# Optimization experiments

Measured on AMD Instinct MI355X. Metric: run time of the kernel, lower is better.

## Reference

```python
import jax, jax.numpy as jnp
import numpy as np

N = 50000      # nodes
E = 800000     # edges (before self loops)
D_IN = 128
HID = 64
HEADS = 8
D_OUT = 10


def setup_inputs() -> dict:
    key = jax.random.key(0)
    ks = jax.random.split(key, 16)
    sc = 0.05
    x = jax.random.normal(ks[0], (N, D_IN), dtype=jnp.float32)
    edge_index = jax.random.randint(ks[1], (2, E), 0, N, dtype=jnp.int64)
    return {
        "x": x,
        "edge_index": edge_index,
        "W1": jax.random.normal(ks[2], (HEADS * HID, D_IN), dtype=jnp.float32) * sc,
        "a1_src": jax.random.normal(ks[3], (HEADS, HID), dtype=jnp.float32) * sc,
        "a1_dst": jax.random.normal(ks[4], (HEADS, HID), dtype=jnp.float32) * sc,
        "b1": jnp.zeros((HEADS * HID,), jnp.float32),
        "W2": jax.random.normal(ks[5], (HID, HEADS * HID), dtype=jnp.float32) * sc,
        "a2_src": jax.random.normal(ks[6], (1, HID), dtype=jnp.float32) * sc,
        "a2_dst": jax.random.normal(ks[7], (1, HID), dtype=jnp.float32) * sc,
        "b2": jnp.zeros((HID,), jnp.float32),
        "W3": jax.random.normal(ks[8], (HID, HID), dtype=jnp.float32) * sc,
        "a3_src": jax.random.normal(ks[9], (1, HID), dtype=jnp.float32) * sc,
        "a3_dst": jax.random.normal(ks[10], (1, HID), dtype=jnp.float32) * sc,
        "b3": jnp.zeros((HID,), jnp.float32),
        "Wc": jax.random.normal(ks[11], (D_OUT, HID), dtype=jnp.float32) * sc,
        "bc": jnp.zeros((D_OUT,), jnp.float32),
    }


def gat_conv(x, src, dst, W, a_src, a_dst, b, concat):
    """PyG GATConv (eval mode, add_self_loops already applied to src/dst)."""
    heads, out_ch = a_src.shape
    n = x.shape[0]
    h = (x @ W.T).reshape(n, heads, out_ch)          # [N, H, C]
    a_s = jnp.einsum('nhc,hc->nh', h, a_src)          # [N, H]
    a_d = jnp.einsum('nhc,hc->nh', h, a_dst)          # [N, H]
    e = jax.nn.leaky_relu(a_s[src] + a_d[dst], 0.2)   # [Etot, H]
    # segment softmax over incoming edges of each destination node
    m = jax.ops.segment_max(e, dst, num_segments=n)
    ex = jnp.exp(e - m[dst])
    s = jax.ops.segment_sum(ex, dst, num_segments=n)
    alpha = ex / (s[dst] + 1e-16)                     # [Etot, H]
    out = jax.ops.segment_sum(h[src] * alpha[:, :, None], dst, num_segments=n)
    if concat:
        out = out.reshape(n, heads * out_ch)
    else:
        out = out.mean(axis=1)
    return out + b


def reference(x, edge_index, W1, a1_src, a1_dst, b1, W2, a2_src, a2_dst, b2,
              W3, a3_src, a3_dst, b3, Wc, bc):
    loops = jnp.arange(N, dtype=edge_index.dtype)
    src = jnp.concatenate([edge_index[0], loops])
    dst = jnp.concatenate([edge_index[1], loops])
    h = jax.nn.elu(gat_conv(x, src, dst, W1, a1_src, a1_dst, b1, True))
    h = jax.nn.elu(gat_conv(h, src, dst, W2, a2_src, a2_dst, b2, False))
    h = jax.nn.elu(gat_conv(h, src, dst, W3, a3_src, a3_dst, b3, False))
    return h @ Wc.T + bc
```

## Files before the change

### kernel.cpp

```cpp
#include <hip/hip_runtime.h>
#include <math.h>

#define N_NODES 50000
#define N_EDGES 800000
#define ETOT    (N_EDGES + N_NODES)

typedef short bf16x8 __attribute__((ext_vector_type(8)));
typedef float f32x4  __attribute__((ext_vector_type(4)));

__device__ __forceinline__ float b2f(unsigned int u16) {
    return __uint_as_float(u16 << 16);
}
__device__ __forceinline__ unsigned short f2b(float f) {
    unsigned int u = __float_as_uint(f);
    u += 0x7fffu + ((u >> 16) & 1u);
    return (unsigned short)(u >> 16);
}
__device__ __forceinline__ void unpack8(uint4 v, float* f) {
    f[0] = __uint_as_float(v.x << 16); f[1] = __uint_as_float(v.x & 0xffff0000u);
    f[2] = __uint_as_float(v.y << 16); f[3] = __uint_as_float(v.y & 0xffff0000u);
    f[4] = __uint_as_float(v.z << 16); f[5] = __uint_as_float(v.z & 0xffff0000u);
    f[6] = __uint_as_float(v.w << 16); f[7] = __uint_as_float(v.w & 0xffff0000u);
}

__global__ __launch_bounds__(256) void k_prep(const float* __restrict__ w1,
                                              const float* __restrict__ w2,
                                              const float* __restrict__ w3,
                                              unsigned short* __restrict__ o1,
                                              unsigned short* __restrict__ o2,
                                              unsigned short* __restrict__ o3,
                                              int* __restrict__ deg,
                                              int* __restrict__ flag) {
    int i = blockIdx.x * 256 + threadIdx.x;
    if (i < N_NODES) deg[i] = 0;
    if (i == 0) *flag = 0;
    if (i < 512 * 128 / 4) {
        float4 v = ((const float4*)w1)[i];
        ushort2* o = (ushort2*)(o1 + i * 4);
        o[0] = make_ushort2(f2b(v.x), f2b(v.y));
        o[1] = make_ushort2(f2b(v.z), f2b(v.w));
    }
    if (i < 64 * 512 / 4) {
        float4 v = ((const float4*)w2)[i];
        ushort2* o = (ushort2*)(o2 + i * 4);
        o[0] = make_ushort2(f2b(v.x), f2b(v.y));
        o[1] = make_ushort2(f2b(v.z), f2b(v.w));
    }
    if (i < 64 * 64 / 4) {
        float4 v = ((const float4*)w3)[i];
        ushort2* o = (ushort2*)(o3 + i * 4);
        o[0] = make_ushort2(f2b(v.x), f2b(v.y));
        o[1] = make_ushort2(f2b(v.z), f2b(v.w));
    }
}

__global__ void k_detect(const int* __restrict__ idx, int* __restrict__ flag) {
    int i = blockIdx.x * blockDim.x + threadIdx.x;
    int v = idx[2 * i + 1];
    unsigned long long any = __ballot(v != 0);
    if ((threadIdx.x & 63) == 0 && any) atomicOr(flag, 1);
}

__device__ __forceinline__ int edge_src(const int* idx, int e, int is32) {
    return is32 ? idx[e] : idx[2 * e];
}
__device__ __forceinline__ int edge_dst(const int* idx, int e, int is32) {
    return is32 ? idx[N_EDGES + e] : idx[2 * (N_EDGES + e)];
}

__global__ void k_degree(const int* __restrict__ idx, const int* __restrict__ flag,
                         int* __restrict__ deg) {
    int e = blockIdx.x * blockDim.x + threadIdx.x;
    if (e >= ETOT) return;
    int is32 = *flag;
    int d = (e < N_EDGES) ? edge_dst(idx, e, is32) : (e - N_EDGES);
    atomicAdd(&deg[d], 1);
}

__global__ __launch_bounds__(256) void k_scan1(const int* __restrict__ deg,
                                               int* __restrict__ rowptr,
                                               int* __restrict__ bsum) {
    __shared__ int sd[256];
    int t = threadIdx.x;
    int i = blockIdx.x * 256 + t;
    int v = (i < N_NODES) ? deg[i] : 0;
    sd[t] = v;
    __syncthreads();
#pragma unroll
    for (int off = 1; off < 256; off <<= 1) {
        int a = (t >= off) ? sd[t - off] : 0;
        __syncthreads();
        sd[t] += a;
        __syncthreads();
    }
    if (i < N_NODES) rowptr[i] = sd[t] - v;
    if (t == 255) bsum[blockIdx.x] = sd[255];
}

__global__ __launch_bounds__(256) void k_scan2(int* __restrict__ bsum,
                                               int* __restrict__ boff,
                                               int* __restrict__ rowptr,
                                               int nb) {
    __shared__ int sd[256];
    int t = threadIdx.x;
    int v = (t < nb) ? bsum[t] : 0;
    sd[t] = v;
    __syncthreads();
#pragma unroll
    for (int off = 1; off < 256; off <<= 1) {
        int a = (t >= off) ? sd[t - off] : 0;
        __syncthreads();
        sd[t] += a;
        __syncthreads();
    }
    boff[t] = sd[t] - v;
    if (t == 255) rowptr[N_NODES] = sd[255];
}

__global__ __launch_bounds__(256) void k_scan3(int* __restrict__ rowptr,
                                               const int* __restrict__ boff,
                                               int* __restrict__ cursor) {
    int i = blockIdx.x * 256 + threadIdx.x;
    if (i >= N_NODES) return;
    int r = rowptr[i] + boff[blockIdx.x];
    rowptr[i] = r;
    cursor[i] = r;
}

__global__ void k_scatter(const int* __restrict__ idx, const int* __restrict__ flag,
                          int* __restrict__ cursor, int* __restrict__ col) {
    int e = blockIdx.x * blockDim.x + threadIdx.x;
    if (e >= ETOT) return;
    int is32 = *flag;
    int s, d;
    if (e < N_EDGES) { s = edge_src(idx, e, is32); d = edge_dst(idx, e, is32); }
    else             { s = d = e - N_EDGES; }
    int pos = atomicAdd(&cursor[d], 1);
    col[pos] = s;
}

template<int AFP32>
__global__ __launch_bounds__(256) void k_gemm(const float* __restrict__ Af,
                                              const unsigned short* __restrict__ Ab,
                                              const unsigned short* __restrict__ W,
                                              unsigned short* __restrict__ C,
                                              const float* __restrict__ a_src,
                                              const float* __restrict__ a_dst,
                                              float* __restrict__ asb,
                                              float* __restrict__ adb,
                                              int M, int K, int Nout, int Hstr) {
    __shared__ unsigned short As[64 * 40];
    __shared__ unsigned short Bs[64 * 40];
    __shared__ float red_s[4][64];
    __shared__ float red_d[4][64];
    int t = threadIdx.x;
    int w = t >> 6, l = t & 63;
    int quad = l >> 4, lm = l & 15;
    int m0 = blockIdx.y * 64, n0 = blockIdx.x * 64;
    int hd = blockIdx.x;
    int lr = t >> 2;
    int lc = (t & 3) * 8;

    f32x4 acc[4];
#pragma unroll
    for (int r = 0; r < 4; ++r) acc[r] = (f32x4){0.f, 0.f, 0.f, 0.f};

    for (int k0 = 0; k0 < K; k0 += 32) {
        int m = m0 + lr;
        if (AFP32) {
            float4 a0 = {0.f,0.f,0.f,0.f}, a1 = {0.f,0.f,0.f,0.f};
            if (m < M) {
                const float4* ap = (const float4*)(Af + (size_t)m * K + k0 + lc);
                a0 = ap[0]; a1 = ap[1];
            }
            unsigned int u0 = (unsigned int)f2b(a0.x) | ((unsigned int)f2b(a0.y) << 16);
            unsigned int u1 = (unsigned int)f2b(a0.z) | ((unsigned int)f2b(a0.w) << 16);
            unsigned int u2 = (unsigned int)f2b(a1.x) | ((unsigned int)f2b(a1.y) << 16);
            unsigned int u3 = (unsigned int)f2b(a1.z) | ((unsigned int)f2b(a1.w) << 16);
            *(uint4*)&As[lr * 40 + lc] = make_uint4(u0, u1, u2, u3);
        } else {
            uint4 av = make_uint4(0, 0, 0, 0);
            if (m < M) av = *(const uint4*)(Ab + (size_t)m * K + k0 + lc);
            *(uint4*)&As[lr * 40 + lc] = av;
        }
        uint4 bv = *(const uint4*)(W + (size_t)(n0 + lr) * K + k0 + lc);
        *(uint4*)&Bs[lr * 40 + lc] = bv;
        __syncthreads();

        bf16x8 bfrag = *(const bf16x8*)&Bs[(w * 16 + lm) * 40 + quad * 8];
#pragma unroll
        for (int r = 0; r < 4; ++r) {
            bf16x8 afrag = *(const bf16x8*)&As[(r * 16 + lm) * 40 + quad * 8];
            acc[r] = __builtin_amdgcn_mfma_f32_16x16x32_bf16(afrag, bfrag, acc[r], 0, 0, 0);
        }
        __syncthreads();
    }

#pragma unroll
    for (int r = 0; r < 4; ++r)
#pragma unroll
        for (int g = 0; g < 4; ++g) {
            int m = m0 + r * 16 + quad * 4 + g;
            if (m < M) C[(size_t)m * Nout + n0 + w * 16 + lm] = f2b(acc[r][g]);
        }

    float as = a_src[hd * 64 + w * 16 + lm];
    float ad = a_dst[hd * 64 + w * 16 + lm];
#pragma unroll
    for (int r = 0; r < 4; ++r) {
#pragma unroll
        for (int g = 0; g < 4; ++g) {
            float vs = acc[r][g] * as;
            float vd = acc[r][g] * ad;
#pragma unroll
            for (int off = 1; off < 16; off <<= 1) {
                vs += __shfl_xor(vs, off);
                vd += __shfl_xor(vd, off);
            }
            if (lm == 0) {
                red_s[w][r * 16 + quad * 4 + g] = vs;
                red_d[w][r * 16 + quad * 4 + g] = vd;
            }
        }
    }
    __syncthreads();
    if (t < 64) {
        float vs = red_s[0][t] + red_s[1][t] + red_s[2][t] + red_s[3][t];
        float vd = red_d[0][t] + red_d[1][t] + red_d[2][t] + red_d[3][t];
        int m = m0 + t;
        if (m < M) {
            asb[(size_t)m * Hstr + hd] = vs;
            adb[(size_t)m * Hstr + hd] = vd;
        }
    }
}

__global__ __launch_bounds__(256) void k_agg8(const unsigned short* __restrict__ h,
                                              const float* __restrict__ asrc,
                                              const float* __restrict__ adst,
                                              const int* __restrict__ rowptr,
                                              const int* __restrict__ col,
                                              const float* __restrict__ bias,
                                              unsigned short* __restrict__ out) {
    int n = blockIdx.x * 4 + (threadIdx.x >> 6);
    if (n >= N_NODES) return;
    int l = threadIdx.x & 63;
    int j = l >> 3;
    int start = rowptr[n], end = rowptr[n + 1];
    float adn = adst[n * 8 + j];

    float ssum = 0.f;
    float o[8] = {0.f, 0.f, 0.f, 0.f, 0.f, 0.f, 0.f, 0.f};
    int k = start;
    for (; k + 4 <= end; k += 4) {
        int s0 = col[k], s1 = col[k + 1], s2 = col[k + 2], s3 = col[k + 3];
        float t0 = asrc[s0 * 8 + j], t1 = asrc[s1 * 8 + j];
        float t2 = asrc[s2 * 8 + j], t3 = asrc[s3 * 8 + j];
        uint4 hv0 = *(const uint4*)(h + (size_t)s0 * 512 + l * 8);
        uint4 hv1 = *(const uint4*)(h + (size_t)s1 * 512 + l * 8);
        uint4 hv2 = *(const uint4*)(h + (size_t)s2 * 512 + l * 8);
        uint4 hv3 = *(const uint4*)(h + (size_t)s3 * 512 + l * 8);
        float f[8];
        float e0 = t0 + adn; e0 = (e0 > 0.f) ? e0 : 0.2f * e0;
        float ex0 = __expf(e0); ssum += ex0;
        unpack8(hv0, f);
#pragma unroll
        for (int i = 0; i < 8; ++i) o[i] += ex0 * f[i];
        float e1 = t1 + adn; e1 = (e1 > 0.f) ? e1 : 0.2f * e1;
        float ex1 = __expf(e1); ssum += ex1;
        unpack8(hv1, f);
#pragma unroll
        for (int i = 0; i < 8; ++i) o[i] += ex1 * f[i];
        float e2 = t2 + adn; e2 = (e2 > 0.f) ? e2 : 0.2f * e2;
        float ex2 = __expf(e2); ssum += ex2;
        unpack8(hv2, f);
#pragma unroll
        for (int i = 0; i < 8; ++i) o[i] += ex2 * f[i];
        float e3 = t3 + adn; e3 = (e3 > 0.f) ? e3 : 0.2f * e3;
        float ex3 = __expf(e3); ssum += ex3;
        unpack8(hv3, f);
#pragma unroll
        for (int i = 0; i < 8; ++i) o[i] += ex3 * f[i];
    }
    for (; k < end; ++k) {
        int s = col[k];
        float e = asrc[s * 8 + j] + adn;
        e = (e > 0.f) ? e : 0.2f * e;
        float ex = __expf(e);
        ssum += ex;
        uint4 hv = *(const uint4*)(h + (size_t)s * 512 + l * 8);
        float f[8];
        unpack8(hv, f);
#pragma unroll
        for (int i = 0; i < 8; ++i) o[i] += ex * f[i];
    }
    float inv = 1.f / (ssum + 1e-16f);
    unsigned int p[4];
#pragma unroll
    for (int i = 0; i < 4; ++i) {
        float v0 = o[2 * i] * inv + bias[l * 8 + 2 * i];
        float v1 = o[2 * i + 1] * inv + bias[l * 8 + 2 * i + 1];
        v0 = (v0 > 0.f) ? v0 : expm1f(v0);
        v1 = (v1 > 0.f) ? v1 : expm1f(v1);
        p[i] = (unsigned int)f2b(v0) | ((unsigned int)f2b(v1) << 16);
    }
    *(uint4*)(out + (size_t)n * 512 + l * 8) = make_uint4(p[0], p[1], p[2], p[3]);
}

__global__ __launch_bounds__(256) void k_agg1(const unsigned short* __restrict__ h,
                                              const float* __restrict__ asrc,
                                              const float* __restrict__ adst,
                                              const int* __restrict__ rowptr,
                                              const int* __restrict__ col,
                                              const float* __restrict__ bias,
                                              unsigned short* __restrict__ out) {
    int n = blockIdx.x * 4 + (threadIdx.x >> 6);
    if (n >= N_NODES) return;
    int l = threadIdx.x & 63;
    int start = rowptr[n], end = rowptr[n + 1];
    float adn = adst[n];

    float ssum = 0.f, o = 0.f;
    int k = start;
    for (; k + 4 <= end; k += 4) {
        int s0 = col[k], s1 = col[k + 1], s2 = col[k + 2], s3 = col[k + 3];
        float t0 = asrc[s0], t1 = asrc[s1], t2 = asrc[s2], t3 = asrc[s3];
        unsigned short q0 = h[(size_t)s0 * 64 + l];
        unsigned short q1 = h[(size_t)s1 * 64 + l];
        unsigned short q2 = h[(size_t)s2 * 64 + l];
        unsigned short q3 = h[(size_t)s3 * 64 + l];
        float e0 = t0 + adn; e0 = (e0 > 0.f) ? e0 : 0.2f * e0;
        float ex0 = __expf(e0); ssum += ex0; o += ex0 * b2f(q0);
        float e1 = t1 + adn; e1 = (e1 > 0.f) ? e1 : 0.2f * e1;
        float ex1 = __expf(e1); ssum += ex1; o += ex1 * b2f(q1);
        float e2 = t2 + adn; e2 = (e2 > 0.f) ? e2 : 0.2f * e2;
        float ex2 = __expf(e2); ssum += ex2; o += ex2 * b2f(q2);
        float e3 = t3 + adn; e3 = (e3 > 0.f) ? e3 : 0.2f * e3;
        float ex3 = __expf(e3); ssum += ex3; o += ex3 * b2f(q3);
    }
    for (; k < end; ++k) {
        int s = col[k];
        float e = asrc[s] + adn;
        e = (e > 0.f) ? e : 0.2f * e;
        float ex = __expf(e);
        ssum += ex;
        o += ex * b2f(h[(size_t)s * 64 + l]);
    }
    float v = o / (ssum + 1e-16f) + bias[l];
    v = (v > 0.f) ? v : expm1f(v);
    out[(size_t)n * 64 + l] = f2b(v);
}

__global__ __launch_bounds__(256) void k_classifier(const unsigned short* __restrict__ h,
                                                    const float* __restrict__ Wc,
                                                    const float* __restrict__ bc,
                                                    float* __restrict__ out) {
    __shared__ float sW[640];
    for (int i = threadIdx.x; i < 640; i += blockDim.x) sW[i] = Wc[i];
    __syncthreads();
    int idx = blockIdx.x * blockDim.x + threadIdx.x;
    if (idx >= N_NODES * 10) return;
    int n = idx / 10, d = idx - n * 10;
    const unsigned short* hr = h + (size_t)n * 64;
    const float* wr = sW + d * 64;
    float acc = 0.f;
#pragma unroll
    for (int c = 0; c < 64; ++c) acc += b2f(hr[c]) * wr[c];
    out[idx] = acc + bc[d];
}

extern "C" void kernel_launch(void* const* d_in, const int* in_sizes, int n_in,
                              void* d_out, int out_size, void* d_ws, size_t ws_size,
                              hipStream_t stream) {
    const float* x    = (const float*)d_in[0];
    const int*   eidx = (const int*)  d_in[1];
    const float* W1   = (const float*)d_in[2];
    const float* a1s  = (const float*)d_in[3];
    const float* a1d  = (const float*)d_in[4];
    const float* b1   = (const float*)d_in[5];
    const float* W2   = (const float*)d_in[6];
    const float* a2s  = (const float*)d_in[7];
    const float* a2d  = (const float*)d_in[8];
    const float* b2   = (const float*)d_in[9];
    const float* W3   = (const float*)d_in[10];
    const float* a3s  = (const float*)d_in[11];
    const float* a3d  = (const float*)d_in[12];
    const float* b3   = (const float*)d_in[13];
    const float* Wc   = (const float*)d_in[14];
    const float* bc   = (const float*)d_in[15];
    float* out = (float*)d_out;

    float* asbuf = (float*)d_ws;
    float* adbuf = asbuf + (size_t)N_NODES * 8;
    unsigned short* h1  = (unsigned short*)(adbuf + (size_t)N_NODES * 8);
    unsigned short* x2  = h1  + (size_t)N_NODES * 512;
    unsigned short* h2  = x2  + (size_t)N_NODES * 512;
    unsigned short* x3  = h2  + (size_t)N_NODES * 64;
    unsigned short* h3  = x3  + (size_t)N_NODES * 64;
    unsigned short* x4  = h3  + (size_t)N_NODES * 64;
    unsigned short* W1b = x4  + (size_t)N_NODES * 64;
    unsigned short* W2b = W1b + 512 * 128;
    unsigned short* W3b = W2b + 64 * 512;
    int* ibase  = (int*)(W3b + 64 * 64);
    int* deg    = ibase;
    int* flag   = deg + N_NODES;
    int* rowptr = flag + 1;
    int* cursor = rowptr + N_NODES + 1;
    int* bsum   = cursor + N_NODES;
    int* boff   = bsum + 256;
    int* col    = boff + 256;

    dim3 blk(256);
    const int SCAN_BLOCKS = (N_NODES + 255) / 256;

    k_prep<<<SCAN_BLOCKS, blk, 0, stream>>>(W1, W2, W3, W1b, W2b, W3b, deg, flag);
    k_detect<<<32, blk, 0, stream>>>(eidx, flag);
    k_degree<<<(ETOT + 255) / 256, blk, 0, stream>>>(eidx, flag, deg);
    k_scan1<<<SCAN_BLOCKS, blk, 0, stream>>>(deg, rowptr, bsum);
    k_scan2<<<1, blk, 0, stream>>>(bsum, boff, rowptr, SCAN_BLOCKS);
    k_scan3<<<SCAN_BLOCKS, blk, 0, stream>>>(rowptr, boff, cursor);
    k_scatter<<<(ETOT + 255) / 256, blk, 0, stream>>>(eidx, flag, cursor, col);

    int mblocks = (N_NODES + 63) / 64;
    int nblocks = N_NODES / 4;

    k_gemm<1><<<dim3(8, mblocks), blk, 0, stream>>>(x, (const unsigned short*)0, W1b, h1,
                                                    a1s, a1d, asbuf, adbuf,
                                                    N_NODES, 128, 512, 8);
    k_agg8<<<nblocks, blk, 0, stream>>>(h1, asbuf, adbuf, rowptr, col, b1, x2);

    k_gemm<0><<<dim3(1, mblocks), blk, 0, stream>>>((const float*)0, x2, W2b, h2,
                                                    a2s, a2d, asbuf, adbuf,
                                                    N_NODES, 512, 64, 1);
    k_agg1<<<nblocks, blk, 0, stream>>>(h2, asbuf, adbuf, rowptr, col, b2, x3);

    k_gemm<0><<<dim3(1, mblocks), blk, 0, stream>>>((const float*)0, x3, W3b, h3,
                                                    a3s, a3d, asbuf, adbuf,
                                                    N_NODES, 64, 64, 1);
    k_agg1<<<nblocks, blk, 0, stream>>>(h3, asbuf, adbuf, rowptr, col, b3, x4);

    k_classifier<<<(N_NODES * 10 + 255) / 256, blk, 0, stream>>>(x4, Wc, bc, out);
}
```

Before: 507.5 us.

## Pre-convert x to bf16, vectorize col loads, use packed FMA in aggregation

The input features are converted to bf16 once in the prep kernel, so the first GEMM reads bf16 instead of converting fp32 on the fly across 8 column blocks. The aggregation kernels now align the edge loop and load column indices as int4 with a one-step prefetch, use 32-bit unsigned index arithmetic, and use fmaxf for leaky-relu. The 8-head aggregation accumulates with v_pk_fma_f32 inline asm. These target gather latency and ALU work in the memory-bound aggregation, at the cost of an extra bf16 copy of x in the workspace and a larger prep launch.

Result: no change. 512.7 us (+1.0%).

```diff
diff --git a/kernel.cpp b/kernel.cpp
--- a/kernel.cpp
+++ b/kernel.cpp
@@ -7,6 +7,7 @@
 
 typedef short bf16x8 __attribute__((ext_vector_type(8)));
 typedef float f32x4  __attribute__((ext_vector_type(4)));
+typedef float f32x2  __attribute__((ext_vector_type(2)));
 
 __device__ __forceinline__ float b2f(unsigned int u16) {
     return __uint_as_float(u16 << 16);
@@ -16,16 +17,12 @@
     u += 0x7fffu + ((u >> 16) & 1u);
     return (unsigned short)(u >> 16);
 }
-__device__ __forceinline__ void unpack8(uint4 v, float* f) {
-    f[0] = __uint_as_float(v.x << 16); f[1] = __uint_as_float(v.x & 0xffff0000u);
-    f[2] = __uint_as_float(v.y << 16); f[3] = __uint_as_float(v.y & 0xffff0000u);
-    f[4] = __uint_as_float(v.z << 16); f[5] = __uint_as_float(v.z & 0xffff0000u);
-    f[6] = __uint_as_float(v.w << 16); f[7] = __uint_as_float(v.w & 0xffff0000u);
-}
-
-__global__ __launch_bounds__(256) void k_prep(const float* __restrict__ w1,
+
+__global__ __launch_bounds__(256) void k_prep(const float* __restrict__ x,
+                                              const float* __restrict__ w1,
                                               const float* __restrict__ w2,
                                               const float* __restrict__ w3,
+                                              unsigned short* __restrict__ xb,
                                               unsigned short* __restrict__ o1,
                                               unsigned short* __restrict__ o2,
                                               unsigned short* __restrict__ o3,
@@ -51,6 +48,15 @@
         ushort2* o = (ushort2*)(o3 + i * 4);
         o[0] = make_ushort2(f2b(v.x), f2b(v.y));
         o[1] = make_ushort2(f2b(v.z), f2b(v.w));
+    }
+    if (i < N_NODES * 128 / 8) {
+        const float4* xp = (const float4*)x + (size_t)i * 2;
+        float4 v0 = xp[0], v1 = xp[1];
+        unsigned int u0 = (unsigned int)f2b(v0.x) | ((unsigned int)f2b(v0.y) << 16);
+        unsigned int u1 = (unsigned int)f2b(v0.z) | ((unsigned int)f2b(v0.w) << 16);
+        unsigned int u2 = (unsigned int)f2b(v1.x) | ((unsigned int)f2b(v1.y) << 16);
+        unsigned int u3 = (unsigned int)f2b(v1.z) | ((unsigned int)f2b(v1.w) << 16);
+        *(uint4*)(xb + (size_t)i * 8) = make_uint4(u0, u1, u2, u3);
     }
 }
 
@@ -235,6 +241,24 @@
     }
 }
 
+__device__ __forceinline__ void agg8_acc(float t, float adn, uint4 hv,
+                                         float& ssum, f32x2* o2) {
+    float e = t + adn;
+    e = fmaxf(e, 0.2f * e);
+    float ex = __expf(e);
+    ssum += ex;
+    f32x2 ex2 = {ex, ex};
+    f32x2 f;
+    f.x = __uint_as_float(hv.x << 16); f.y = __uint_as_float(hv.x & 0xffff0000u);
+    asm("v_pk_fma_f32 %0, %1, %2, %0" : "+v"(o2[0]) : "v"(f), "v"(ex2));
+    f.x = __uint_as_float(hv.y << 16); f.y = __uint_as_float(hv.y & 0xffff0000u);
+    asm("v_pk_fma_f32 %0, %1, %2, %0" : "+v"(o2[1]) : "v"(f), "v"(ex2));
+    f.x = __uint_as_float(hv.z << 16); f.y = __uint_as_float(hv.z & 0xffff0000u);
+    asm("v_pk_fma_f32 %0, %1, %2, %0" : "+v"(o2[2]) : "v"(f), "v"(ex2));
+    f.x = __uint_as_float(hv.w << 16); f.y = __uint_as_float(hv.w & 0xffff0000u);
+    asm("v_pk_fma_f32 %0, %1, %2, %0" : "+v"(o2[3]) : "v"(f), "v"(ex2));
+}
+
 __global__ __launch_bounds__(256) void k_agg8(const unsigned short* __restrict__ h,
                                               const float* __restrict__ asrc,
                                               const float* __restrict__ adst,
@@ -246,65 +270,62 @@
     if (n >= N_NODES) return;
     int l = threadIdx.x & 63;
     int j = l >> 3;
+    int lbase = l << 3;
     int start = rowptr[n], end = rowptr[n + 1];
-    float adn = adst[n * 8 + j];
+    float adn = adst[(n << 3) + j];
 
     float ssum = 0.f;
-    float o[8] = {0.f, 0.f, 0.f, 0.f, 0.f, 0.f, 0.f, 0.f};
+    f32x2 o2[4];
+#pragma unroll
+    for (int i = 0; i < 4; ++i) o2[i] = (f32x2){0.f, 0.f};
+
     int k = start;
-    for (; k + 4 <= end; k += 4) {
-        int s0 = col[k], s1 = col[k + 1], s2 = col[k + 2], s3 = col[k + 3];
-        float t0 = asrc[s0 * 8 + j], t1 = asrc[s1 * 8 + j];
-        float t2 = asrc[s2 * 8 + j], t3 = asrc[s3 * 8 + j];
-        uint4 hv0 = *(const uint4*)(h + (size_t)s0 * 512 + l * 8);
-        uint4 hv1 = *(const uint4*)(h + (size_t)s1 * 512 + l * 8);
-        uint4 hv2 = *(const uint4*)(h + (size_t)s2 * 512 + l * 8);
-        uint4 hv3 = *(const uint4*)(h + (size_t)s3 * 512 + l * 8);
-        float f[8];
-        float e0 = t0 + adn; e0 = (e0 > 0.f) ? e0 : 0.2f * e0;
-        float ex0 = __expf(e0); ssum += ex0;
-        unpack8(hv0, f);
-#pragma unroll
-        for (int i = 0; i < 8; ++i) o[i] += ex0 * f[i];
-        float e1 = t1 + adn; e1 = (e1 > 0.f) ? e1 : 0.2f * e1;
-        float ex1 = __expf(e1); ssum += ex1;
-        unpack8(hv1, f);
-#pragma unroll
-        for (int i = 0; i < 8; ++i) o[i] += ex1 * f[i];
-        float e2 = t2 + adn; e2 = (e2 > 0.f) ? e2 : 0.2f * e2;
-        float ex2 = __expf(e2); ssum += ex2;
-        unpack8(hv2, f);
-#pragma unroll
-        for (int i = 0; i < 8; ++i) o[i] += ex2 * f[i];
-        float e3 = t3 + adn; e3 = (e3 > 0.f) ? e3 : 0.2f * e3;
-        float ex3 = __expf(e3); ssum += ex3;
-        unpack8(hv3, f);
-#pragma unroll
-        for (int i = 0; i < 8; ++i) o[i] += ex3 * f[i];
+    int kA = (start + 3) & ~3;
+    if (kA > end) kA = end;
+    for (; k < kA; ++k) {
+        int s = col[k];
+        float t = asrc[((unsigned)s << 3) + (unsigned)j];
+        uint4 hv = *(const uint4*)(h + ((unsigned)s << 9) + (unsigned)lbase);
+        agg8_acc(t, adn, hv, ssum, o2);
+    }
+    int kEnd4 = kA + ((end - kA) & ~3);
+    if (k < kEnd4) {
+        int4 cN = *(const int4*)(col + k);
+        for (; k < kEnd4; k += 4) {
+            int4 c = cN;
+            if (k + 8 <= kEnd4) cN = *(const int4*)(col + k + 4);
+            float t0 = asrc[((unsigned)c.x << 3) + (unsigned)j];
+            float t1 = asrc[((unsigned)c.y << 3) + (unsigned)j];
+            float t2 = asrc[((unsigned)c.z << 3) + (unsigned)j];
+            float t3 = asrc[((unsigned)c.w << 3) + (unsigned)j];
+            uint4 hv0 = *(const uint4*)(h + ((unsigned)c.x << 9) + (unsigned)lbase);
+            uint4 hv1 = *(const uint4*)(h + ((unsigned)c.y << 9) + (unsigned)lbase);
+            uint4 hv2 = *(const uint4*)(h + ((unsigned)c.z << 9) + (unsigned)lbase);
+            uint4 hv3 = *(const uint4*)(h + ((unsigned)c.w << 9) + (unsigned)lbase);
+            agg8_acc(t0, adn, hv0, ssum, o2);
+            agg8_acc(t1, adn, hv1, ssum, o2);
+            agg8_acc(t2, adn, hv2, ssum, o2);
+            agg8_acc(t3, adn, hv3, ssum, o2);
+        }
     }
     for (; k < end; ++k) {
         int s = col[k];
-        float e = asrc[s * 8 + j] + adn;
-        e = (e > 0.f) ? e : 0.2f * e;
-        float ex = __expf(e);
-        ssum += ex;
-        uint4 hv = *(const uint4*)(h + (size_t)s * 512 + l * 8);
-        float f[8];
-        unpack8(hv, f);
-#pragma unroll
-        for (int i = 0; i < 8; ++i) o[i] += ex * f[i];
-    }
+        float t = asrc[((unsigned)s << 3) + (unsigned)j];
+        uint4 hv = *(const uint4*)(h + ((unsigned)s << 9) + (unsigned)lbase);
+        agg8_acc(t, adn, hv, ssum, o2);
+    }
+
     float inv = 1.f / (ssum + 1e-16f);
     unsigned int p[4];
 #pragma unroll
     for (int i = 0; i < 4; ++i) {
-        float v0 = o[2 * i] * inv + bias[l * 8 + 2 * i];
-        float v1 = o[2 * i + 1] * inv + bias[l * 8 + 2 * i + 1];
+        float v0 = o2[i].x * inv + bias[lbase + 2 * i];
+        float v1 = o2[i].y * inv + bias[lbase + 2 * i + 1];
         v0 = (v0 > 0.f) ? v0 : expm1f(v0);
         v1 = (v1 > 0.f) ? v1 : expm1f(v1);
         p[i] = (unsigned int)f2b(v0) | ((unsigned int)f2b(v1) << 16);
     }
-    *(uint4*)(out + (size_t)n * 512 + l * 8) = make_uint4(p[0], p[1], p[2], p[3]);
+    *(uint4*)(out + (size_t)n * 512 + lbase) = make_uint4(p[0], p[1], p[2], p[3]);
 }
 
 __global__ __launch_bounds__(256) void k_agg1(const unsigned short* __restrict__ h,
@@ -322,29 +343,44 @@
 
     float ssum = 0.f, o = 0.f;
     int k = start;
-    for (; k + 4 <= end; k += 4) {
-        int s0 = col[k], s1 = col[k + 1], s2 = col[k + 2], s3 = col[k + 3];
-        float t0 = asrc[s0], t1 = asrc[s1], t2 = asrc[s2], t3 = asrc[s3];
-        unsigned short q0 = h[(size_t)s0 * 64 + l];
-        unsigned short q1 = h[(size_t)s1 * 64 + l];
-        unsigned short q2 = h[(size_t)s2 * 64 + l];
-        unsigned short q3 = h[(size_t)s3 * 64 + l];
-        float e0 = t0 + adn; e0 = (e0 > 0.f) ? e0 : 0.2f * e0;
-        float ex0 = __expf(e0); ssum += ex0; o += ex0 * b2f(q0);
-        float e1 = t1 + adn; e1 = (e1 > 0.f) ? e1 : 0.2f * e1;
-        float ex1 = __expf(e1); ssum += ex1; o += ex1 * b2f(q1);
-        float e2 = t2 + adn; e2 = (e2 > 0.f) ? e2 : 0.2f * e2;
-        float ex2 = __expf(e2); ssum += ex2; o += ex2 * b2f(q2);
-        float e3 = t3 + adn; e3 = (e3 > 0.f) ? e3 : 0.2f * e3;
-        float ex3 = __expf(e3); ssum += ex3; o += ex3 * b2f(q3);
+    int kA = (start + 3) & ~3;
+    if (kA > end) kA = end;
+    for (; k < kA; ++k) {
+        int s = col[k];
+        float t = asrc[s];
+        float hf = b2f(h[((unsigned)s << 6) + (unsigned)l]);
+        float e = t + adn; e = fmaxf(e, 0.2f * e);
+        float ex = __expf(e);
+        ssum += ex; o += ex * hf;
+    }
+    int kEnd4 = kA + ((end - kA) & ~3);
+    if (k < kEnd4) {
+        int4 cN = *(const int4*)(col + k);
+        for (; k < kEnd4; k += 4) {
+            int4 c = cN;
+            if (k + 8 <= kEnd4) cN = *(const int4*)(col + k + 4);
+            float t0 = asrc[c.x], t1 = asrc[c.y], t2 = asrc[c.z], t3 = asrc[c.w];
+            unsigned short q0 = h[((unsigned)c.x << 6) + (unsigned)l];
+            unsigned short q1 = h[((unsigned)c.y << 6) + (unsigned)l];
+            unsigned short q2 = h[((unsigned)c.z << 6) + (unsigned)l];
+            unsigned short q3 = h[((unsigned)c.w << 6) + (unsigned)l];
+            float e0 = t0 + adn; e0 = fmaxf(e0, 0.2f * e0);
+            float ex0 = __expf(e0); ssum += ex0; o += ex0 * b2f(q0);
+            float e1 = t1 + adn; e1 = fmaxf(e1, 0.2f * e1);
+            float ex1 = __expf(e1); ssum += ex1; o += ex1 * b2f(q1);
+            float e2 = t2 + adn; e2 = fmaxf(e2, 0.2f * e2);
+            float ex2 = __expf(e2); ssum += ex2; o += ex2 * b2f(q2);
+            float e3 = t3 + adn; e3 = fmaxf(e3, 0.2f * e3);
+            float ex3 = __expf(e3); ssum += ex3; o += ex3 * b2f(q3);
+        }
     }
     for (; k < end; ++k) {
         int s = col[k];
-        float e = asrc[s] + adn;
-        e = (e > 0.f) ? e : 0.2f * e;
+        float t = asrc[s];
+        float hf = b2f(h[((unsigned)s << 6) + (unsigned)l]);
+        float e = t + adn; e = fmaxf(e, 0.2f * e);
         float ex = __expf(e);
-        ssum += ex;
-        o += ex * b2f(h[(size_t)s * 64 + l]);
+        ssum += ex; o += ex * hf;
     }
     float v = o / (ssum + 1e-16f) + bias[l];
     v = (v > 0.f) ? v : expm1f(v);
@@ -398,7 +434,8 @@
     unsigned short* x3  = h2  + (size_t)N_NODES * 64;
     unsigned short* h3  = x3  + (size_t)N_NODES * 64;
     unsigned short* x4  = h3  + (size_t)N_NODES * 64;
-    unsigned short* W1b = x4  + (size_t)N_NODES * 64;
+    unsigned short* xb  = x4  + (size_t)N_NODES * 64;
+    unsigned short* W1b = xb  + (size_t)N_NODES * 128;
     unsigned short* W2b = W1b + 512 * 128;
     unsigned short* W3b = W2b + 64 * 512;
     int* ibase  = (int*)(W3b + 64 * 64);
@@ -412,8 +449,9 @@
 
     dim3 blk(256);
     const int SCAN_BLOCKS = (N_NODES + 255) / 256;
-
-    k_prep<<<SCAN_BLOCKS, blk, 0, stream>>>(W1, W2, W3, W1b, W2b, W3b, deg, flag);
+    const int PREP_BLOCKS = (N_NODES * 128 / 8 + 255) / 256;
+
+    k_prep<<<PREP_BLOCKS, blk, 0, stream>>>(x, W1, W2, W3, xb, W1b, W2b, W3b, deg, flag);
     k_detect<<<32, blk, 0, stream>>>(eidx, flag);
     k_degree<<<(ETOT + 255) / 256, blk, 0, stream>>>(eidx, flag, deg);
     k_scan1<<<SCAN_BLOCKS, blk, 0, stream>>>(deg, rowptr, bsum);
@@ -424,7 +462,7 @@
     int mblocks = (N_NODES + 63) / 64;
     int nblocks = N_NODES / 4;
 
-    k_gemm<1><<<dim3(8, mblocks), blk, 0, stream>>>(x, (const unsigned short*)0, W1b, h1,
+    k_gemm<0><<<dim3(8, mblocks), blk, 0, stream>>>((const float*)0, xb, W1b, h1,
                                                     a1s, a1d, asbuf, adbuf,
                                                     N_NODES, 128, 512, 8);
     k_agg8<<<nblocks, blk, 0, stream>>>(h1, asbuf, adbuf, rowptr, col, b1, x2);
```
